# Kernel tuning notes

Measured on AMD Instinct MI355X. Metric: run time of the kernel, lower is better.

Reference implementation:

```python
import jax, jax.numpy as jnp
import numpy as np

N = 65536      # batch of CPU-state samples
D = 64         # byte-embedding dim
H = 512        # expert hidden dim
V = 256        # byte vocabulary / result logits
NFLAGS = 8
# number of embedded inputs per expert
KS = {"alu": 4, "logic": 4, "move": 5, "flow": 6, "stack": 6}


def setup_inputs() -> dict:
    key = jax.random.key(0)
    ks = list(jax.random.split(key, 64))
    nk = lambda: ks.pop()
    rint = lambda mx: jax.random.randint(nk(), (N,), 0, mx, dtype=jnp.int32)
    inp = {n: rint(256) for n in ["A", "X", "Y", "SP", "P", "PCH", "PCL", "Op", "Val"]}
    # deterministic opcode -> functional-unit map (stand-in for build_fu_map)
    inp["fu_map"] = (jnp.arange(256, dtype=jnp.int32) % 5)
    p = lambda shape: jax.random.normal(nk(), shape, dtype=jnp.float32) * 0.02
    for name, k in KS.items():
        inp[f"{name}_emb"] = p((k, V, D))
        inp[f"{name}_W1"] = p((k * D, H))
        inp[f"{name}_b1"] = jnp.zeros((H,), jnp.float32)
    inp["alu_Wr"] = p((H, V)); inp["alu_Wf"] = p((H, NFLAGS))
    inp["logic_Wr"] = p((H, V)); inp["logic_Wf"] = p((H, NFLAGS))
    inp["move_Wo"] = p((H, V))
    inp["flow_Wo"] = p((H, V))
    inp["stack_Wo"] = p((H, V))
    return inp


def _expert_hidden(emb, idx_list, W1, b1):
    # emb: [k, 256, D]; idx_list: k arrays of [N] byte indices
    ids = jnp.stack(idx_list)                                  # [k, N]
    f = emb[jnp.arange(emb.shape[0])[:, None], ids]            # [k, N, D] gather
    f = jnp.moveaxis(f, 0, 1).reshape(ids.shape[1], -1)        # [N, k*D]
    return jax.nn.gelu(f @ W1 + b1)                            # [N, H]


def reference(A, X, Y, SP, P, PCH, PCL, Op, Val, fu_map,
              alu_emb, alu_W1, alu_b1, alu_Wr, alu_Wf,
              logic_emb, logic_W1, logic_b1, logic_Wr, logic_Wf,
              move_emb, move_W1, move_b1, move_Wo,
              flow_emb, flow_W1, flow_b1, flow_Wo,
              stack_emb, stack_W1, stack_b1, stack_Wo):
    # deterministic zero-cost router: opcode -> FU id
    fu = fu_map[Op]                                            # [N]
    carry = P & 1                                              # carry bit of status reg
    mask = lambda k: (fu == k)[:, None].astype(jnp.float32)
    # ALU (FU 0): a, operand, carry, opcode -> result + flags logits
    h = _expert_hidden(alu_emb, [A, Val, carry, Op], alu_W1, alu_b1)
    alu = jnp.concatenate([h @ alu_Wr, h @ alu_Wf], -1) * mask(0)      # [N, 264]
    # LOGIC (FU 1): same inputs, separate params
    h = _expert_hidden(logic_emb, [A, Val, carry, Op], logic_W1, logic_b1)
    logic = jnp.concatenate([h @ logic_Wr, h @ logic_Wf], -1) * mask(1)  # [N, 264]
    # MOVE (FU 2): a, x, y, operand, opcode
    move = (_expert_hidden(move_emb, [A, X, Y, Val, Op], move_W1, move_b1) @ move_Wo) * mask(2)
    # FLOW (FU 3): pc (as PCH,PCL bytes), flags, target, sp, opcode
    flow = (_expert_hidden(flow_emb, [PCH, PCL, P, Val, SP, Op], flow_W1, flow_b1) @ flow_Wo) * mask(3)
    # STACK (FU 4): a, x, sp, flags, stack_top, opcode
    stack = (_expert_hidden(stack_emb, [A, X, SP, P, Val, Op], stack_W1, stack_b1) @ stack_Wo) * mask(4)
    # dense capacity-1 dispatch: each sample's row is nonzero only in its FU's slice
    return jnp.concatenate([alu, logic, move, flow, stack], -1)        # [N, 1296]
```

## Files before the change

### kernel.cpp

```cpp
#include <hip/hip_runtime.h>

#define DEV __device__ __forceinline__

typedef __attribute__((ext_vector_type(8))) short short8;
typedef __attribute__((ext_vector_type(4))) float f32x4;
typedef unsigned short u16;

struct Ptrs { const void* p[32]; };

constexpr int N_TOK = 65536;
constexpr int cK  [5] = {4,4,5,6,6};
constexpr int cK1 [5] = {256,256,320,384,384};
constexpr int cN2 [5] = {264,264,256,256,256};
constexpr int cNT [5] = {17,17,16,16,16};
constexpr int cC0 [5] = {0,264,528,784,1040};
constexpr int cKID[5][6] = {{0,8,9,7,0,0},{0,8,9,7,0,0},{0,1,2,8,7,0},
                            {5,6,4,8,3,7},{0,1,3,4,8,7}};
constexpr int cEOFF[5] = {0,65536,131072,212992,311296};
constexpr int cWOFF[5] = {0,131072,262144,425984,622592};
constexpr int cHOFF[5] = {0,139264,278528,417792,557056};
constexpr int EMB_TOT = 409600, W1_TOT = 819200, HEAD_TOT = 696320;
constexpr int PREP_TOT = EMB_TOT + W1_TOT + HEAD_TOT;

constexpr size_t WS_COUNTS = 0;
constexpr size_t WS_BUCKET = 256;
constexpr size_t WS_EMB    = 256 + (size_t)5 * N_TOK * 4;
constexpr size_t WS_W1T    = WS_EMB + (size_t)EMB_TOT * 2;
constexpr size_t WS_HT     = WS_W1T + (size_t)W1_TOT * 2;

constexpr int ROWS = 128;
constexpr int HP   = 520;

constexpr int TOK_OFF = ROWS * HP * 2;
constexpr int IDS_OFF = TOK_OFF + ROWS * 4;
constexpr int LDS_BYTES = IDS_OFF + ROWS * 6 * 4;

DEV u16 f2bf(float f) {
  unsigned u = __builtin_bit_cast(unsigned, f);
  u += 0x7FFFu + ((u >> 16) & 1u);
  return (u16)(u >> 16);
}

DEV float gelu_f(float x) {
  float u = 0.7978845608028654f * x * (1.0f + 0.044715f * x * x);
  float t2 = fminf(fmaxf(2.0f * u, -30.0f), 30.0f);
  float e = __expf(t2);
  float th = (e - 1.0f) / (e + 1.0f);
  return 0.5f * x * (1.0f + th);
}

__global__ __launch_bounds__(256) void prep_kernel(Ptrs in, u16* embB, u16* w1tB, u16* hTB) {
  int idx = blockIdx.x * 256 + threadIdx.x;
  if (idx < EMB_TOT) {
    int e = 0, off = idx;
    while (off >= cK[e] * 16384) { off -= cK[e] * 16384; ++e; }
    const float* src = (const float*)in.p[10 + 3*e];
    embB[cEOFF[e] + off] = f2bf(src[off]);
  } else if (idx < EMB_TOT + W1_TOT) {
    int off = idx - EMB_TOT;
    int e = 0;
    while (off >= 512 * cK1[e]) { off -= 512 * cK1[e]; ++e; }
    int K1 = cK1[e];
    int n = off / K1, k = off - n * K1;
    const float* w1 = (const float*)in.p[11 + 3*e];
    w1tB[cWOFF[e] + off] = f2bf(w1[k * 512 + n]);
  } else {
    int off = idx - (EMB_TOT + W1_TOT);
    int e = off / 139264, r = off - e * 139264;
    int n = r >> 9, k = r & 511;
    float v = 0.0f;
    if (e < 2) {
      if (n < 256)       v = ((const float*)in.p[25 + 2*e])[k * 256 + n];
      else if (n < 264)  v = ((const float*)in.p[26 + 2*e])[k * 8 + (n - 256)];
    } else {
      if (n < 256)       v = ((const float*)in.p[29 + (e - 2)])[k * 256 + n];
    }
    hTB[cHOFF[e] + r] = f2bf(v);
  }
}

__global__ __launch_bounds__(256) void bucket_kernel(const int* Op, const int* fu_map,
                                                     int* counts, int* buckets) {
  __shared__ int lc[5], lb[5];
  int tid = threadIdx.x;
  if (tid < 5) lc[tid] = 0;
  __syncthreads();
  int t = blockIdx.x * 256 + tid;
  int fu = fu_map[Op[t]];
  int lp = atomicAdd(&lc[fu], 1);
  __syncthreads();
  if (tid < 5) lb[tid] = atomicAdd(&counts[tid], lc[tid]);
  __syncthreads();
  buckets[fu * N_TOK + lb[fu] + lp] = t;
}

template<int E>
DEV void expert_tile(const Ptrs& in, int tile, int count, const int* buckets,
                     const u16* embB, const u16* w1tB, const u16* hTB,
                     float* out, char* smem) {
  constexpr int K1 = cK1[E], KT = cK1[E] / 32, N2 = cN2[E], C0 = cC0[E];
  constexpr int NT = cNT[E], KE = cK[E];
  constexpr int FB  = K1 * 2;
  constexpr int CPR = KE * 8;

  u16* hbuf = (u16*)smem;
  int* tokb = (int*)(smem + TOK_OFF);
  int* idsb = (int*)(smem + IDS_OFF);

  const int tid = threadIdx.x;
  const int vr = min(count - tile * ROWS, ROWS);
  const int rbase = E * N_TOK + tile * ROWS;

  __syncthreads();

  if (tid < ROWS)
    tokb[tid] = (tid < vr) ? buckets[rbase + tid] : -1;
  for (int i = tid; i < ROWS * KE; i += 512) {
    int r = i / KE, k = i - r * KE;
    int t = buckets[rbase + ((r < vr) ? r : 0)];
    int s = cKID[E][k];
    int v = (s == 9) ? (((const int*)in.p[4])[t] & 1)
                     : ((const int*)in.p[s])[t];
    idsb[r * 6 + k] = v;
  }
  __syncthreads();

  const int lane = tid & 63, wave = tid >> 6;
  const int l15 = lane & 15, lq = (lane >> 4) & 3;

  {
    constexpr int ZC  = (1296 - N2) / 4;
    constexpr int ZLO = C0 / 4;
    constexpr int ZHI = (C0 + N2) / 4;
    const f32x4 z4 = {0.f, 0.f, 0.f, 0.f};
    for (int r = wave; r < vr; r += 8) {
      float* rowp = out + (size_t)tokb[r] * 1296;
      #pragma unroll
      for (int c = 0; c < ZC; c += 64) {
        int cc = c + lane;
        if (cc < ZC) {
          int col4 = (cc < ZLO) ? cc : (cc - ZLO + ZHI);
          __builtin_nontemporal_store(z4, (f32x4*)(rowp + col4 * 4));
        }
      }
    }
  }

  {
    const u16* embE = embB + cEOFF[E];
    short8 val[KT];
    int    dst[KT];
    #pragma unroll
    for (int it = 0; it < KT; ++it) {
      int d = tid + it * 512;
      int r = d / CPR, c = d - r * CPR;
      int k = c >> 3;
      int id = idsb[r * 6 + k];
      val[it] = *(const short8*)(embE + (size_t)((k * 256 + id) << 6) + ((c & 7) << 3));
      dst[it] = r * FB + ((c * 16) ^ ((r & 7) << 4));
    }
    #pragma unroll
    for (int it = 0; it < KT; ++it)
      *(short8*)(smem + dst[it]) = val[it];
  }
  __syncthreads();

  const u16* w1e  = w1tB + cWOFF[E];
  const float* b1 = (const float*)in.p[12 + 3 * E];

  f32x4 acc[8][4];
  {
    const f32x4 z = {0.f, 0.f, 0.f, 0.f};
    #pragma unroll
    for (int m = 0; m < 8; ++m)
      #pragma unroll
      for (int nt = 0; nt < 4; ++nt) acc[m][nt] = z;
  }
  #pragma unroll 2
  for (int kt = 0; kt < KT; ++kt) {
    short8 a[8], b[4];
    #pragma unroll
    for (int m = 0; m < 8; ++m) {
      int row = m * 16 + l15;
      a[m] = *(const short8*)(smem + row * FB + ((kt * 64 + lq * 16) ^ ((row & 7) << 4)));
    }
    #pragma unroll
    for (int nt = 0; nt < 4; ++nt)
      b[nt] = *(const short8*)(w1e + (wave * 64 + nt * 16 + l15) * K1 + kt * 32 + lq * 8);
    #pragma unroll
    for (int nt = 0; nt < 4; ++nt)
      #pragma unroll
      for (int m = 0; m < 8; ++m)
        acc[m][nt] = __builtin_amdgcn_mfma_f32_16x16x32_bf16(a[m], b[nt], acc[m][nt], 0, 0, 0);
  }
  __syncthreads();

  #pragma unroll
  for (int nt = 0; nt < 4; ++nt) {
    int col = wave * 64 + nt * 16 + l15;
    float b1v = b1[col];
    #pragma unroll
    for (int m = 0; m < 8; ++m)
      #pragma unroll
      for (int q = 0; q < 4; ++q)
        hbuf[(m * 16 + lq * 4 + q) * HP + col] = f2bf(gelu_f(acc[m][nt][q] + b1v));
  }
  __syncthreads();

  const u16* hTe = hTB + cHOFF[E];
  f32x4 acc2[8][3];
  {
    const f32x4 z = {0.f, 0.f, 0.f, 0.f};
    #pragma unroll
    for (int m = 0; m < 8; ++m)
      #pragma unroll
      for (int j = 0; j < 3; ++j) acc2[m][j] = z;
  }
  #pragma unroll 4
  for (int kt = 0; kt < 16; ++kt) {
    short8 a[8];
    #pragma unroll
    for (int m = 0; m < 8; ++m)
      a[m] = *(const short8*)(hbuf + (m * 16 + l15) * HP + kt * 32 + lq * 8);
    #pragma unroll
    for (int j = 0; j < 3; ++j) {
      int nt = wave + 8 * j;
      if (nt >= NT) break;
      short8 b = *(const short8*)(hTe + (nt * 16 + l15) * 512 + kt * 32 + lq * 8);
      #pragma unroll
      for (int m = 0; m < 8; ++m)
        acc2[m][j] = __builtin_amdgcn_mfma_f32_16x16x32_bf16(a[m], b, acc2[m][j], 0, 0, 0);
    }
  }

  int trow[8][4];
  #pragma unroll
  for (int m = 0; m < 8; ++m)
    #pragma unroll
    for (int q = 0; q < 4; ++q)
      trow[m][q] = tokb[m * 16 + lq * 4 + q];

  #pragma unroll
  for (int j = 0; j < 3; ++j) {
    int nt = wave + 8 * j;
    if (nt >= NT) break;
    int coln = nt * 16 + l15;
    if (coln < N2) {
      #pragma unroll
      for (int m = 0; m < 8; ++m)
        #pragma unroll
        for (int q = 0; q < 4; ++q) {
          int t = trow[m][q];
          if (t >= 0)
            __builtin_nontemporal_store(acc2[m][j][q],
                                        out + (size_t)t * 1296 + C0 + coln);
        }
    }
  }
}

__global__ __launch_bounds__(512, 2) void moe_kernel(Ptrs in, const int* counts,
                                                     const int* buckets,
                                                     const u16* embB, const u16* w1tB,
                                                     const u16* hTB, float* out) {
  extern __shared__ char smem[];
  int c0 = counts[0], c1 = counts[1], c2 = counts[2], c3 = counts[3], c4 = counts[4];
  int t0 = (c0 + ROWS - 1) / ROWS;
  int t1 = (c1 + ROWS - 1) / ROWS;
  int t2 = (c2 + ROWS - 1) / ROWS;
  int t3 = (c3 + ROWS - 1) / ROWS;
  int t4 = (c4 + ROWS - 1) / ROWS;
  int p1 = t0, p2 = p1 + t1, p3 = p2 + t2, p4 = p3 + t3, p5 = p4 + t4;

  const int x = blockIdx.x & 7;
  const int slot = blockIdx.x >> 3;
  const int beg = (x * p5) >> 3;
  const int end = ((x + 1) * p5) >> 3;

  for (int g = beg + slot; g < end; g += 64) {
    int e = 0, base = 0, cnt = c0;
    if (g >= p1) { e = 1; base = p1; cnt = c1; }
    if (g >= p2) { e = 2; base = p2; cnt = c2; }
    if (g >= p3) { e = 3; base = p3; cnt = c3; }
    if (g >= p4) { e = 4; base = p4; cnt = c4; }
    int tile = g - base;
    switch (e) {
      case 0: expert_tile<0>(in, tile, cnt, buckets, embB, w1tB, hTB, out, smem); break;
      case 1: expert_tile<1>(in, tile, cnt, buckets, embB, w1tB, hTB, out, smem); break;
      case 2: expert_tile<2>(in, tile, cnt, buckets, embB, w1tB, hTB, out, smem); break;
      case 3: expert_tile<3>(in, tile, cnt, buckets, embB, w1tB, hTB, out, smem); break;
      case 4: expert_tile<4>(in, tile, cnt, buckets, embB, w1tB, hTB, out, smem); break;
    }
  }
}

extern "C" void kernel_launch(void* const* d_in, const int* in_sizes, int n_in,
                              void* d_out, int out_size, void* d_ws, size_t ws_size,
                              hipStream_t stream) {
  char* ws = (char*)d_ws;
  int* counts  = (int*)(ws + WS_COUNTS);
  int* buckets = (int*)(ws + WS_BUCKET);
  u16* embB    = (u16*)(ws + WS_EMB);
  u16* w1tB    = (u16*)(ws + WS_W1T);
  u16* hTB     = (u16*)(ws + WS_HT);

  Ptrs P;
  for (int i = 0; i < 32; ++i) P.p[i] = d_in[i];

  (void)hipMemsetAsync(counts, 0, 5 * sizeof(int), stream);
  prep_kernel<<<PREP_TOT / 256, 256, 0, stream>>>(P, embB, w1tB, hTB);
  bucket_kernel<<<N_TOK / 256, 256, 0, stream>>>((const int*)d_in[7], (const int*)d_in[9],
                                                 counts, buckets);
  moe_kernel<<<512, 512, LDS_BYTES, stream>>>(P, counts, buckets, embB, w1tB, hTB,
                                              (float*)d_out);
}
```

Before: 236.5 us.

## Stage expert outputs in compact buffer and expand with separate coalesced kernel

Expert tiles now write results into LDS and then store them contiguously into a compact per-token workspace buffer, instead of scattering stores and zero-fills into the wide output. A new expand kernel reads the compact buffer and writes each full 1296-column output row, inserting zeros outside the token's expert slice. This aims to make output writes sequential and coalesced, at the cost of an extra intermediate buffer round-trip and kernel launch. The larger LDS footprint also reduces the moe kernel to one block per CU.

```diff
diff --git a/kernel.cpp b/kernel.cpp
--- a/kernel.cpp
+++ b/kernel.cpp
@@ -27,13 +27,16 @@
 constexpr size_t WS_EMB    = 256 + (size_t)5 * N_TOK * 4;
 constexpr size_t WS_W1T    = WS_EMB + (size_t)EMB_TOT * 2;
 constexpr size_t WS_HT     = WS_W1T + (size_t)W1_TOT * 2;
+constexpr size_t WS_COMP   = WS_HT + (size_t)HEAD_TOT * 2;
+constexpr int    COMP_STRIDE = 272;
 
 constexpr int ROWS = 128;
 constexpr int HP   = 520;
 
-constexpr int TOK_OFF = ROWS * HP * 2;
-constexpr int IDS_OFF = TOK_OFF + ROWS * 4;
-constexpr int LDS_BYTES = IDS_OFF + ROWS * 6 * 4;
+constexpr int TOK_OFF = 0;
+constexpr int IDS_OFF = 512;
+constexpr int BUF_OFF = 3584;
+constexpr int LDS_BYTES = BUF_OFF + 135168;
 
 DEV u16 f2bf(float f) {
   unsigned u = __builtin_bit_cast(unsigned, f);
@@ -97,15 +100,16 @@
 template<int E>
 DEV void expert_tile(const Ptrs& in, int tile, int count, const int* buckets,
                      const u16* embB, const u16* w1tB, const u16* hTB,
-                     float* out, char* smem) {
-  constexpr int K1 = cK1[E], KT = cK1[E] / 32, N2 = cN2[E], C0 = cC0[E];
+                     float* comp, char* smem) {
+  constexpr int K1 = cK1[E], KT = cK1[E] / 32, N2 = cN2[E];
   constexpr int NT = cNT[E], KE = cK[E];
   constexpr int FB  = K1 * 2;
   constexpr int CPR = KE * 8;
 
-  u16* hbuf = (u16*)smem;
-  int* tokb = (int*)(smem + TOK_OFF);
-  int* idsb = (int*)(smem + IDS_OFF);
+  u16*   hbuf = (u16*)(smem + BUF_OFF);
+  float* rbuf = (float*)(smem + BUF_OFF);
+  int*   tokb = (int*)(smem + TOK_OFF);
+  int*   idsb = (int*)(smem + IDS_OFF);
 
   const int tid = threadIdx.x;
   const int vr = min(count - tile * ROWS, ROWS);
@@ -129,24 +133,6 @@
   const int l15 = lane & 15, lq = (lane >> 4) & 3;
 
   {
-    constexpr int ZC  = (1296 - N2) / 4;
-    constexpr int ZLO = C0 / 4;
-    constexpr int ZHI = (C0 + N2) / 4;
-    const f32x4 z4 = {0.f, 0.f, 0.f, 0.f};
-    for (int r = wave; r < vr; r += 8) {
-      float* rowp = out + (size_t)tokb[r] * 1296;
-      #pragma unroll
-      for (int c = 0; c < ZC; c += 64) {
-        int cc = c + lane;
-        if (cc < ZC) {
-          int col4 = (cc < ZLO) ? cc : (cc - ZLO + ZHI);
-          __builtin_nontemporal_store(z4, (f32x4*)(rowp + col4 * 4));
-        }
-      }
-    }
-  }
-
-  {
     const u16* embE = embB + cEOFF[E];
     short8 val[KT];
     int    dst[KT];
@@ -157,7 +143,7 @@
       int k = c >> 3;
       int id = idsb[r * 6 + k];
       val[it] = *(const short8*)(embE + (size_t)((k * 256 + id) << 6) + ((c & 7) << 3));
-      dst[it] = r * FB + ((c * 16) ^ ((r & 7) << 4));
+      dst[it] = BUF_OFF + r * FB + ((c * 16) ^ ((r & 7) << 4));
     }
     #pragma unroll
     for (int it = 0; it < KT; ++it)
@@ -182,7 +168,8 @@
     #pragma unroll
     for (int m = 0; m < 8; ++m) {
       int row = m * 16 + l15;
-      a[m] = *(const short8*)(smem + row * FB + ((kt * 64 + lq * 16) ^ ((row & 7) << 4)));
+      a[m] = *(const short8*)(smem + BUF_OFF + row * FB +
+                              ((kt * 64 + lq * 16) ^ ((row & 7) << 4)));
     }
     #pragma unroll
     for (int nt = 0; nt < 4; ++nt)
@@ -232,13 +219,7 @@
         acc2[m][j] = __builtin_amdgcn_mfma_f32_16x16x32_bf16(a[m], b, acc2[m][j], 0, 0, 0);
     }
   }
-
-  int trow[8][4];
-  #pragma unroll
-  for (int m = 0; m < 8; ++m)
-    #pragma unroll
-    for (int q = 0; q < 4; ++q)
-      trow[m][q] = tokb[m * 16 + lq * 4 + q];
+  __syncthreads();
 
   #pragma unroll
   for (int j = 0; j < 3; ++j) {
@@ -249,20 +230,28 @@
       #pragma unroll
       for (int m = 0; m < 8; ++m)
         #pragma unroll
-        for (int q = 0; q < 4; ++q) {
-          int t = trow[m][q];
-          if (t >= 0)
-            __builtin_nontemporal_store(acc2[m][j][q],
-                                        out + (size_t)t * 1296 + C0 + coln);
-        }
-    }
-  }
-}
-
-__global__ __launch_bounds__(512, 2) void moe_kernel(Ptrs in, const int* counts,
+        for (int q = 0; q < 4; ++q)
+          rbuf[(m * 16 + lq * 4 + q) * N2 + coln] = acc2[m][j][q];
+    }
+  }
+  __syncthreads();
+
+  {
+    constexpr int V = N2 / 4;
+    int tot = vr * V;
+    for (int idx = tid; idx < tot; idx += 512) {
+      int r = idx / V, c = idx - r * V;
+      int t = tokb[r];
+      f32x4 v = *(const f32x4*)(rbuf + r * N2 + c * 4);
+      __builtin_nontemporal_store(v, (f32x4*)(comp + (size_t)t * COMP_STRIDE + c * 4));
+    }
+  }
+}
+
+__global__ __launch_bounds__(512, 1) void moe_kernel(Ptrs in, const int* counts,
                                                      const int* buckets,
                                                      const u16* embB, const u16* w1tB,
-                                                     const u16* hTB, float* out) {
+                                                     const u16* hTB, float* comp) {
   extern __shared__ char smem[];
   int c0 = counts[0], c1 = counts[1], c2 = counts[2], c3 = counts[3], c4 = counts[4];
   int t0 = (c0 + ROWS - 1) / ROWS;
@@ -285,11 +274,33 @@
     if (g >= p4) { e = 4; base = p4; cnt = c4; }
     int tile = g - base;
     switch (e) {
-      case 0: expert_tile<0>(in, tile, cnt, buckets, embB, w1tB, hTB, out, smem); break;
-      case 1: expert_tile<1>(in, tile, cnt, buckets, embB, w1tB, hTB, out, smem); break;
-      case 2: expert_tile<2>(in, tile, cnt, buckets, embB, w1tB, hTB, out, smem); break;
-      case 3: expert_tile<3>(in, tile, cnt, buckets, embB, w1tB, hTB, out, smem); break;
-      case 4: expert_tile<4>(in, tile, cnt, buckets, embB, w1tB, hTB, out, smem); break;
+      case 0: expert_tile<0>(in, tile, cnt, buckets, embB, w1tB, hTB, comp, smem); break;
+      case 1: expert_tile<1>(in, tile, cnt, buckets, embB, w1tB, hTB, comp, smem); break;
+      case 2: expert_tile<2>(in, tile, cnt, buckets, embB, w1tB, hTB, comp, smem); break;
+      case 3: expert_tile<3>(in, tile, cnt, buckets, embB, w1tB, hTB, comp, smem); break;
+      case 4: expert_tile<4>(in, tile, cnt, buckets, embB, w1tB, hTB, comp, smem); break;
+    }
+  }
+}
+
+__global__ __launch_bounds__(256) void expand_kernel(const int* Op, const int* fu_map,
+                                                     const float* comp, float* out) {
+  const int lane = threadIdx.x & 63, wv = threadIdx.x >> 6;
+  for (int t = blockIdx.x * 4 + wv; t < N_TOK; t += gridDim.x * 4) {
+    int fu = fu_map[Op[t]];
+    int c0q = cC0[fu] >> 2;
+    int n2q = cN2[fu] >> 2;
+    const float* cr = comp + (size_t)t * COMP_STRIDE;
+    float* orow = out + (size_t)t * 1296;
+    #pragma unroll
+    for (int it = 0; it < 6; ++it) {
+      int c4 = it * 64 + lane;
+      if (c4 < 324) {
+        f32x4 v = {0.f, 0.f, 0.f, 0.f};
+        int rel = c4 - c0q;
+        if (rel >= 0 && rel < n2q) v = *(const f32x4*)(cr + rel * 4);
+        __builtin_nontemporal_store(v, (f32x4*)(orow + c4 * 4));
+      }
     }
   }
 }
@@ -303,6 +314,7 @@
   u16* embB    = (u16*)(ws + WS_EMB);
   u16* w1tB    = (u16*)(ws + WS_W1T);
   u16* hTB     = (u16*)(ws + WS_HT);
+  float* comp  = (float*)(ws + WS_COMP);
 
   Ptrs P;
   for (int i = 0; i < 32; ++i) P.p[i] = d_in[i];
@@ -311,6 +323,7 @@
   prep_kernel<<<PREP_TOT / 256, 256, 0, stream>>>(P, embB, w1tB, hTB);
   bucket_kernel<<<N_TOK / 256, 256, 0, stream>>>((const int*)d_in[7], (const int*)d_in[9],
                                                  counts, buckets);
-  moe_kernel<<<512, 512, LDS_BYTES, stream>>>(P, counts, buckets, embB, w1tB, hTB,
-                                              (float*)d_out);
-}
+  moe_kernel<<<512, 512, LDS_BYTES, stream>>>(P, counts, buckets, embB, w1tB, hTB, comp);
+  expand_kernel<<<2048, 256, 0, stream>>>((const int*)d_in[7], (const int*)d_in[9],
+                                          comp, (float*)d_out);
+}
```

Result: slower. 273.1 us (+15.5%).

## Stage output tile through LDS for coalesced row-wise vector stores

Applied to the files above, without the earlier changes.

The second-GEMM results are first written into a padded LDS buffer that reuses the hidden buffer, then each wave copies whole output rows to global memory with 16-byte vector stores. Before, each value was a scattered 4-byte nontemporal store. Zero-fill stores become regular stores instead of nontemporal ones. The LDS layout is reorganised, with token and id arrays first, and the fp32 result buffer makes the allocation larger. Launch bounds drop to one block per CU, which may cut occupancy and latency hiding.

```diff
diff --git a/kernel.cpp b/kernel.cpp
--- a/kernel.cpp
+++ b/kernel.cpp
@@ -31,9 +31,11 @@
 constexpr int ROWS = 128;
 constexpr int HP   = 520;
 
-constexpr int TOK_OFF = ROWS * HP * 2;
-constexpr int IDS_OFF = TOK_OFF + ROWS * 4;
-constexpr int LDS_BYTES = IDS_OFF + ROWS * 6 * 4;
+constexpr int TOK_OFF = 0;
+constexpr int IDS_OFF = 512;
+constexpr int BUF_OFF = 3584;
+constexpr int BUF_SZ  = ROWS * 268 * 4;
+constexpr int LDS_BYTES = BUF_OFF + BUF_SZ;
 
 DEV u16 f2bf(float f) {
   unsigned u = __builtin_bit_cast(unsigned, f);
@@ -100,12 +102,14 @@
                      float* out, char* smem) {
   constexpr int K1 = cK1[E], KT = cK1[E] / 32, N2 = cN2[E], C0 = cC0[E];
   constexpr int NT = cNT[E], KE = cK[E];
+  constexpr int RP  = N2 + 4;
   constexpr int FB  = K1 * 2;
   constexpr int CPR = KE * 8;
 
-  u16* hbuf = (u16*)smem;
-  int* tokb = (int*)(smem + TOK_OFF);
-  int* idsb = (int*)(smem + IDS_OFF);
+  u16*   hbuf = (u16*)(smem + BUF_OFF);
+  float* rbuf = (float*)(smem + BUF_OFF);
+  int*   tokb = (int*)(smem + TOK_OFF);
+  int*   idsb = (int*)(smem + IDS_OFF);
 
   const int tid = threadIdx.x;
   const int vr = min(count - tile * ROWS, ROWS);
@@ -140,7 +144,7 @@
         int cc = c + lane;
         if (cc < ZC) {
           int col4 = (cc < ZLO) ? cc : (cc - ZLO + ZHI);
-          __builtin_nontemporal_store(z4, (f32x4*)(rowp + col4 * 4));
+          *(f32x4*)(rowp + col4 * 4) = z4;
         }
       }
     }
@@ -157,7 +161,7 @@
       int k = c >> 3;
       int id = idsb[r * 6 + k];
       val[it] = *(const short8*)(embE + (size_t)((k * 256 + id) << 6) + ((c & 7) << 3));
-      dst[it] = r * FB + ((c * 16) ^ ((r & 7) << 4));
+      dst[it] = BUF_OFF + r * FB + ((c * 16) ^ ((r & 7) << 4));
     }
     #pragma unroll
     for (int it = 0; it < KT; ++it)
@@ -182,7 +186,8 @@
     #pragma unroll
     for (int m = 0; m < 8; ++m) {
       int row = m * 16 + l15;
-      a[m] = *(const short8*)(smem + row * FB + ((kt * 64 + lq * 16) ^ ((row & 7) << 4)));
+      a[m] = *(const short8*)(smem + BUF_OFF + row * FB +
+                              ((kt * 64 + lq * 16) ^ ((row & 7) << 4)));
     }
     #pragma unroll
     for (int nt = 0; nt < 4; ++nt)
@@ -232,13 +237,7 @@
         acc2[m][j] = __builtin_amdgcn_mfma_f32_16x16x32_bf16(a[m], b, acc2[m][j], 0, 0, 0);
     }
   }
-
-  int trow[8][4];
-  #pragma unroll
-  for (int m = 0; m < 8; ++m)
-    #pragma unroll
-    for (int q = 0; q < 4; ++q)
-      trow[m][q] = tokb[m * 16 + lq * 4 + q];
+  __syncthreads();
 
   #pragma unroll
   for (int j = 0; j < 3; ++j) {
@@ -249,17 +248,29 @@
       #pragma unroll
       for (int m = 0; m < 8; ++m)
         #pragma unroll
-        for (int q = 0; q < 4; ++q) {
-          int t = trow[m][q];
-          if (t >= 0)
-            __builtin_nontemporal_store(acc2[m][j][q],
-                                        out + (size_t)t * 1296 + C0 + coln);
-        }
-    }
-  }
-}
-
-__global__ __launch_bounds__(512, 2) void moe_kernel(Ptrs in, const int* counts,
+        for (int q = 0; q < 4; ++q)
+          rbuf[(m * 16 + lq * 4 + q) * RP + coln] = acc2[m][j][q];
+    }
+  }
+  __syncthreads();
+
+  {
+    constexpr int V = N2 / 4;
+    for (int r = wave; r < vr; r += 8) {
+      int t = tokb[r];
+      float* dst = out + (size_t)t * 1296 + C0;
+      const float* src = rbuf + r * RP;
+      #pragma unroll
+      for (int c = 0; c < V; c += 64) {
+        int cc = c + lane;
+        if (cc < V)
+          *(f32x4*)(dst + cc * 4) = *(const f32x4*)(src + cc * 4);
+      }
+    }
+  }
+}
+
+__global__ __launch_bounds__(512, 1) void moe_kernel(Ptrs in, const int* counts,
                                                      const int* buckets,
                                                      const u16* embB, const u16* w1tB,
                                                      const u16* hTB, float* out) {
```

Result: slower. 243.0 us (+2.7%).

## Prefetch weight fragments across k-steps and move output zeroing to memset

Applied to the files above, without the earlier changes.

Double-buffers the W1 and head weight fragment loads so the next k-step's global loads are in flight during the current MFMAs, and streams A fragments one row-block at a time. The in-kernel zeroing of off-expert output columns is removed and replaced by a full-output hipMemsetAsync before the kernels. Launch bounds change to one block per CU, giving more registers per thread but lower occupancy. The memset adds extra writes of the expert slices that are later overwritten.

```diff
diff --git a/kernel.cpp b/kernel.cpp
--- a/kernel.cpp
+++ b/kernel.cpp
@@ -31,9 +31,11 @@
 constexpr int ROWS = 128;
 constexpr int HP   = 520;
 
-constexpr int TOK_OFF = ROWS * HP * 2;
-constexpr int IDS_OFF = TOK_OFF + ROWS * 4;
-constexpr int LDS_BYTES = IDS_OFF + ROWS * 6 * 4;
+constexpr int TOK_OFF = 0;
+constexpr int IDS_OFF = 512;
+constexpr int BUF_OFF = 3584;
+constexpr int BUF_SZ  = ROWS * HP * 2;
+constexpr int LDS_BYTES = BUF_OFF + BUF_SZ;
 
 DEV u16 f2bf(float f) {
   unsigned u = __builtin_bit_cast(unsigned, f);
@@ -103,9 +105,9 @@
   constexpr int FB  = K1 * 2;
   constexpr int CPR = KE * 8;
 
-  u16* hbuf = (u16*)smem;
-  int* tokb = (int*)(smem + TOK_OFF);
-  int* idsb = (int*)(smem + IDS_OFF);
+  u16*   hbuf = (u16*)(smem + BUF_OFF);
+  int*   tokb = (int*)(smem + TOK_OFF);
+  int*   idsb = (int*)(smem + IDS_OFF);
 
   const int tid = threadIdx.x;
   const int vr = min(count - tile * ROWS, ROWS);
@@ -125,27 +127,6 @@
   }
   __syncthreads();
 
-  const int lane = tid & 63, wave = tid >> 6;
-  const int l15 = lane & 15, lq = (lane >> 4) & 3;
-
-  {
-    constexpr int ZC  = (1296 - N2) / 4;
-    constexpr int ZLO = C0 / 4;
-    constexpr int ZHI = (C0 + N2) / 4;
-    const f32x4 z4 = {0.f, 0.f, 0.f, 0.f};
-    for (int r = wave; r < vr; r += 8) {
-      float* rowp = out + (size_t)tokb[r] * 1296;
-      #pragma unroll
-      for (int c = 0; c < ZC; c += 64) {
-        int cc = c + lane;
-        if (cc < ZC) {
-          int col4 = (cc < ZLO) ? cc : (cc - ZLO + ZHI);
-          __builtin_nontemporal_store(z4, (f32x4*)(rowp + col4 * 4));
-        }
-      }
-    }
-  }
-
   {
     const u16* embE = embB + cEOFF[E];
     short8 val[KT];
@@ -157,7 +138,7 @@
       int k = c >> 3;
       int id = idsb[r * 6 + k];
       val[it] = *(const short8*)(embE + (size_t)((k * 256 + id) << 6) + ((c & 7) << 3));
-      dst[it] = r * FB + ((c * 16) ^ ((r & 7) << 4));
+      dst[it] = BUF_OFF + r * FB + ((c * 16) ^ ((r & 7) << 4));
     }
     #pragma unroll
     for (int it = 0; it < KT; ++it)
@@ -165,6 +146,9 @@
   }
   __syncthreads();
 
+  const int lane = tid & 63, wave = tid >> 6;
+  const int l15 = lane & 15, lq = (lane >> 4) & 3;
+
   const u16* w1e  = w1tB + cWOFF[E];
   const float* b1 = (const float*)in.p[12 + 3 * E];
 
@@ -176,22 +160,32 @@
       #pragma unroll
       for (int nt = 0; nt < 4; ++nt) acc[m][nt] = z;
   }
-  #pragma unroll 2
-  for (int kt = 0; kt < KT; ++kt) {
-    short8 a[8], b[4];
-    #pragma unroll
-    for (int m = 0; m < 8; ++m) {
-      int row = m * 16 + l15;
-      a[m] = *(const short8*)(smem + row * FB + ((kt * 64 + lq * 16) ^ ((row & 7) << 4)));
-    }
+  {
+    short8 bcur[4], bnxt[4];
     #pragma unroll
     for (int nt = 0; nt < 4; ++nt)
-      b[nt] = *(const short8*)(w1e + (wave * 64 + nt * 16 + l15) * K1 + kt * 32 + lq * 8);
-    #pragma unroll
-    for (int nt = 0; nt < 4; ++nt)
-      #pragma unroll
-      for (int m = 0; m < 8; ++m)
-        acc[m][nt] = __builtin_amdgcn_mfma_f32_16x16x32_bf16(a[m], b[nt], acc[m][nt], 0, 0, 0);
+      bcur[nt] = *(const short8*)(w1e + (wave * 64 + nt * 16 + l15) * K1 + lq * 8);
+    #pragma unroll 2
+    for (int kt = 0; kt < KT; ++kt) {
+      if (kt + 1 < KT) {
+        #pragma unroll
+        for (int nt = 0; nt < 4; ++nt)
+          bnxt[nt] = *(const short8*)(w1e + (wave * 64 + nt * 16 + l15) * K1 + (kt + 1) * 32 + lq * 8);
+      }
+      #pragma unroll
+      for (int m = 0; m < 8; ++m) {
+        int r = m * 16 + l15;
+        short8 a = *(const short8*)(smem + BUF_OFF + r * FB +
+                                    (((kt * 4 + lq) << 4) ^ ((r & 7) << 4)));
+        #pragma unroll
+        for (int nt = 0; nt < 4; ++nt)
+          acc[m][nt] = __builtin_amdgcn_mfma_f32_16x16x32_bf16(a, bcur[nt], acc[m][nt], 0, 0, 0);
+      }
+      if (kt + 1 < KT) {
+        #pragma unroll
+        for (int nt = 0; nt < 4; ++nt) bcur[nt] = bnxt[nt];
+      }
+    }
   }
   __syncthreads();
 
@@ -216,20 +210,38 @@
       #pragma unroll
       for (int j = 0; j < 3; ++j) acc2[m][j] = z;
   }
-  #pragma unroll 4
-  for (int kt = 0; kt < 16; ++kt) {
-    short8 a[8];
-    #pragma unroll
-    for (int m = 0; m < 8; ++m)
-      a[m] = *(const short8*)(hbuf + (m * 16 + l15) * HP + kt * 32 + lq * 8);
+  {
+    short8 b2cur[3], b2nxt[3];
     #pragma unroll
     for (int j = 0; j < 3; ++j) {
       int nt = wave + 8 * j;
-      if (nt >= NT) break;
-      short8 b = *(const short8*)(hTe + (nt * 16 + l15) * 512 + kt * 32 + lq * 8);
-      #pragma unroll
-      for (int m = 0; m < 8; ++m)
-        acc2[m][j] = __builtin_amdgcn_mfma_f32_16x16x32_bf16(a[m], b, acc2[m][j], 0, 0, 0);
+      if (nt < NT)
+        b2cur[j] = *(const short8*)(hTe + (nt * 16 + l15) * 512 + lq * 8);
+    }
+    #pragma unroll 2
+    for (int kt = 0; kt < 16; ++kt) {
+      if (kt < 15) {
+        #pragma unroll
+        for (int j = 0; j < 3; ++j) {
+          int nt = wave + 8 * j;
+          if (nt < NT)
+            b2nxt[j] = *(const short8*)(hTe + (nt * 16 + l15) * 512 + (kt + 1) * 32 + lq * 8);
+        }
+      }
+      #pragma unroll
+      for (int m = 0; m < 8; ++m) {
+        short8 a = *(const short8*)(hbuf + (m * 16 + l15) * HP + kt * 32 + lq * 8);
+        #pragma unroll
+        for (int j = 0; j < 3; ++j) {
+          int nt = wave + 8 * j;
+          if (nt < NT)
+            acc2[m][j] = __builtin_amdgcn_mfma_f32_16x16x32_bf16(a, b2cur[j], acc2[m][j], 0, 0, 0);
+        }
+      }
+      if (kt < 15) {
+        #pragma unroll
+        for (int j = 0; j < 3; ++j) b2cur[j] = b2nxt[j];
+      }
     }
   }
 
@@ -243,23 +255,24 @@
   #pragma unroll
   for (int j = 0; j < 3; ++j) {
     int nt = wave + 8 * j;
-    if (nt >= NT) break;
-    int coln = nt * 16 + l15;
-    if (coln < N2) {
-      #pragma unroll
-      for (int m = 0; m < 8; ++m)
-        #pragma unroll
-        for (int q = 0; q < 4; ++q) {
-          int t = trow[m][q];
-          if (t >= 0)
-            __builtin_nontemporal_store(acc2[m][j][q],
-                                        out + (size_t)t * 1296 + C0 + coln);
-        }
-    }
-  }
-}
-
-__global__ __launch_bounds__(512, 2) void moe_kernel(Ptrs in, const int* counts,
+    if (nt < NT) {
+      int coln = nt * 16 + l15;
+      if (coln < N2) {
+        #pragma unroll
+        for (int m = 0; m < 8; ++m)
+          #pragma unroll
+          for (int q = 0; q < 4; ++q) {
+            int t = trow[m][q];
+            if (t >= 0)
+              __builtin_nontemporal_store(acc2[m][j][q],
+                                          out + (size_t)t * 1296 + C0 + coln);
+          }
+      }
+    }
+  }
+}
+
+__global__ __launch_bounds__(512, 1) void moe_kernel(Ptrs in, const int* counts,
                                                      const int* buckets,
                                                      const u16* embB, const u16* w1tB,
                                                      const u16* hTB, float* out) {
@@ -307,6 +320,7 @@
   Ptrs P;
   for (int i = 0; i < 32; ++i) P.p[i] = d_in[i];
 
+  (void)hipMemsetAsync(d_out, 0, (size_t)out_size * 4, stream);
   (void)hipMemsetAsync(counts, 0, 5 * sizeof(int), stream);
   prep_kernel<<<PREP_TOT / 256, 256, 0, stream>>>(P, embB, w1tB, hTB);
   bucket_kernel<<<N_TOK / 256, 256, 0, stream>>>((const int*)d_in[7], (const int*)d_in[9],
```

Result: slower. 255.1 us (+7.8%).
